# Optimization experiments

Measured on AMD Instinct MI355X. Metric: run time of the kernel, lower is better.

## Reference

```python
import jax, jax.numpy as jnp
import numpy as np

MAX_NUM_LEVELS = 3.5
NUM_LEVELS = 4  # mip levels 0..3 (levels clamped to [0, 2.5])


def affine_grid(matrix, N, H, W):
    # F.affine_grid, align_corners=False. matrix: (N,2,3) -> grid (N,H,W,2) in xy order.
    xs = (jnp.arange(W, dtype=jnp.float32) + 0.5) * (2.0 / W) - 1.0
    ys = (jnp.arange(H, dtype=jnp.float32) + 0.5) * (2.0 / H) - 1.0
    gy, gx = jnp.meshgrid(ys, xs, indexing='ij')
    base = jnp.stack([gx, gy, jnp.ones_like(gx)], axis=-1)  # (H,W,3)
    return jnp.einsum('hwk,nik->nhwi', base, matrix)  # (N,H,W,2)


def grid_sample_border(img, grid):
    # bilinear grid_sample, padding_mode='border', align_corners=False
    N, C, H, W = img.shape
    x = (grid[..., 0] + 1.0) * (W / 2.0) - 0.5
    y = (grid[..., 1] + 1.0) * (H / 2.0) - 0.5
    x0 = jnp.floor(x); y0 = jnp.floor(y)
    tx = x - x0; ty = y - y0
    x0i = jnp.clip(x0.astype(jnp.int32), 0, W - 1)
    x1i = jnp.clip(x0.astype(jnp.int32) + 1, 0, W - 1)
    y0i = jnp.clip(y0.astype(jnp.int32), 0, H - 1)
    y1i = jnp.clip(y0.astype(jnp.int32) + 1, 0, H - 1)
    b = jnp.arange(N)[:, None, None]
    g = lambda yi, xi: img[b, :, yi, xi]  # (N,Ho,Wo,C) gather
    out = (g(y0i, x0i) * ((1 - tx) * (1 - ty))[..., None]
           + g(y0i, x1i) * (tx * (1 - ty))[..., None]
           + g(y1i, x0i) * ((1 - tx) * ty)[..., None]
           + g(y1i, x1i) * (tx * ty)[..., None])
    return jnp.transpose(out, (0, 3, 1, 2))  # (N,C,Ho,Wo)


def blur_downsample(x):
    N, C, H, W = x.shape
    k1 = jnp.array([1., 3., 3., 1.], dtype=x.dtype) / 8.0
    k = k1[:, None] * k1[None, :]
    xp = jnp.pad(x, ((0, 0), (0, 0), (1, 2), (1, 2)), mode='reflect')
    kernel = jnp.broadcast_to(k[None, None], (C, 1, 4, 4))
    return jax.lax.conv_general_dilated(xp, kernel, window_strides=(2, 2), padding='VALID',
                                        feature_group_count=C,
                                        dimension_numbers=('NCHW', 'OIHW', 'NCHW'))


def compute_levels(grid, H, W):
    # per-pixel mip LOD from local stretch of the sampling grid (in source pixel units)
    coords = (grid + 1.0) * 0.5 * jnp.array([W, H], dtype=grid.dtype)  # (N,Ho,Wo,2)
    dx = coords[:, :-1, 1:] - coords[:, :-1, :-1]
    dy = coords[:, 1:, :-1] - coords[:, :-1, :-1]
    scale = jnp.maximum(jnp.linalg.norm(dx, axis=-1), jnp.linalg.norm(dy, axis=-1))
    scale = jnp.pad(scale, ((0, 0), (0, 1), (0, 1)), mode='edge')  # (N,Ho,Wo)
    levels = jnp.log2(jnp.maximum(scale, 1.0))
    return jnp.clip(levels, 0.0, MAX_NUM_LEVELS - 1.0)


def mipmap_warp(img, grid):
    N, C, H, W = img.shape
    levels = compute_levels(grid, H, W)  # (N,Ho,Wo)
    pyr = [img]
    for _ in range(NUM_LEVELS - 1):
        pyr.append(blur_downsample(pyr[-1]))
    samples = jnp.stack([grid_sample_border(p, grid) for p in pyr], axis=0)  # (L,N,C,Ho,Wo)
    ls = jnp.arange(NUM_LEVELS, dtype=levels.dtype)[:, None, None, None]
    w = jnp.clip(1.0 - jnp.abs(levels[None] - ls), 0.0, 1.0)  # trilinear blend weights (L,N,Ho,Wo)
    return jnp.einsum('lnhw,lnchw->nchw', w, samples)


def setup_inputs() -> dict:
    key = jax.random.key(0)
    k1, k2, k3 = jax.random.split(key, 3)
    N, C, H, W, D = 64, 3, 256, 256, 512
    img = jax.random.normal(k1, (N, C, H, W), dtype=jnp.float32)
    features = jax.random.normal(k2, (N, D), dtype=jnp.float32)
    # learned head params (zero-init in torch; small random here so the warp is nontrivial)
    lin_w = jax.random.normal(k3, (4, D), dtype=jnp.float32) * 0.02
    lin_b = jnp.zeros((4,), dtype=jnp.float32)
    return {'img': img, 'features': features, 'lin_w': lin_w, 'lin_b': lin_b}


def reference(img, features, lin_w, lin_b):
    params = features @ lin_w.T + lin_b  # (N,4)
    rot = jnp.tanh(params[:, 0:1]) * jnp.pi
    scale = jnp.exp(params[:, 1:2])
    sx, sy = params[:, 2:3], params[:, 3:4]
    c, s = jnp.cos(rot), jnp.sin(rot)
    matrix = jnp.concatenate([scale * c, -scale * s, sx, scale * s, scale * c, sy], axis=1).reshape(-1, 2, 3)
    affine_params = jnp.concatenate([rot, scale, sx, sy], axis=1)
    N, C, H, W = img.shape
    grid = affine_grid(matrix, N, H, W)
    out = mipmap_warp(img, grid)
    return out, grid, matrix, affine_params
```

## Files before the change

kernel.cpp:

```cpp
#include <hip/hip_runtime.h>
#include <math.h>

#define N_B 64
#define C_CH 3
#define H_IMG 256
#define W_IMG 256
#define D_FEAT 512

#define OUT_OFF_GRID   12582912
#define OUT_OFF_MATRIX 20971520
#define OUT_OFF_AFFINE 20971904

__global__ void params_kernel(const float* __restrict__ features,
                              const float* __restrict__ lin_w,
                              const float* __restrict__ lin_b,
                              float* __restrict__ out_matrix,
                              float* __restrict__ out_affine,
                              float* __restrict__ ws_params)
{
    const int n = blockIdx.x;
    const int t = threadIdx.x;
    const float* f = features + n * D_FEAT;
    float f0 = f[t];
    float f1 = f[t + 256];
    float a0 = f0 * lin_w[0 * D_FEAT + t] + f1 * lin_w[0 * D_FEAT + t + 256];
    float a1 = f0 * lin_w[1 * D_FEAT + t] + f1 * lin_w[1 * D_FEAT + t + 256];
    float a2 = f0 * lin_w[2 * D_FEAT + t] + f1 * lin_w[2 * D_FEAT + t + 256];
    float a3 = f0 * lin_w[3 * D_FEAT + t] + f1 * lin_w[3 * D_FEAT + t + 256];

    __shared__ float red[4][256];
    red[0][t] = a0; red[1][t] = a1; red[2][t] = a2; red[3][t] = a3;
    __syncthreads();
    for (int s = 128; s > 0; s >>= 1) {
        if (t < s) {
            red[0][t] += red[0][t + s];
            red[1][t] += red[1][t + s];
            red[2][t] += red[2][t + s];
            red[3][t] += red[3][t + s];
        }
        __syncthreads();
    }
    if (t == 0) {
        float p0 = red[0][0] + lin_b[0];
        float p1 = red[1][0] + lin_b[1];
        float p2 = red[2][0] + lin_b[2];
        float p3 = red[3][0] + lin_b[3];
        float rot   = tanhf(p0) * 3.14159265358979323846f;
        float scale = expf(p1);
        float c = cosf(rot), s = sinf(rot);
        float m00 = scale * c, m01 = -scale * s, m02 = p2;
        float m10 = scale * s, m11 =  scale * c, m12 = p3;
        out_matrix[n * 6 + 0] = m00;
        out_matrix[n * 6 + 1] = m01;
        out_matrix[n * 6 + 2] = m02;
        out_matrix[n * 6 + 3] = m10;
        out_matrix[n * 6 + 4] = m11;
        out_matrix[n * 6 + 5] = m12;
        out_affine[n * 4 + 0] = rot;
        out_affine[n * 4 + 1] = scale;
        out_affine[n * 4 + 2] = p2;
        out_affine[n * 4 + 3] = p3;
        float lv = log2f(fmaxf(scale, 1.0f));
        lv = fminf(fmaxf(lv, 0.0f), 2.5f);
        ws_params[n * 8 + 0] = m00;
        ws_params[n * 8 + 1] = m01;
        ws_params[n * 8 + 2] = m02;
        ws_params[n * 8 + 3] = m10;
        ws_params[n * 8 + 4] = m11;
        ws_params[n * 8 + 5] = m12;
        ws_params[n * 8 + 6] = lv;
        ws_params[n * 8 + 7] = 0.0f;
    }
}

template<int Hs, int Ws>
__global__ void down_kernel(const float* __restrict__ src, float* __restrict__ dst)
{
    constexpr int Hd = Hs / 2, Wd = Ws / 2;
    constexpr int QUADS = Wd / 4;

    const int idx = blockIdx.x * blockDim.x + threadIdx.x;
    const int t   = idx & (QUADS - 1);
    const int i   = (idx / QUADS) & (Hd - 1);
    const int nc  = idx / (QUADS * Hd);

    const float* __restrict__ s = src + (size_t)nc * Hs * Ws;

    int r[4];
#pragma unroll
    for (int a = 0; a < 4; a++) {
        int q = 2 * i + a - 1;
        if (q < 0) q = -q;
        if (q >= Hs) q = 2 * Hs - 2 - q;
        r[a] = q;
    }
    const int c8 = 8 * t;
    const int li = (t > 0)         ? c8 - 1 : 1;
    const int ri = (t < QUADS - 1) ? c8 + 8 : Ws - 2;

    const float k0 = 0.125f, k1 = 0.375f;
    const float kr[4] = {0.125f, 0.375f, 0.375f, 0.125f};

    float acc0 = 0.f, acc1 = 0.f, acc2 = 0.f, acc3 = 0.f;
#pragma unroll
    for (int a = 0; a < 4; a++) {
        const float* row = s + (size_t)r[a] * Ws;
        float4 A = *(const float4*)(row + c8);
        float4 B = *(const float4*)(row + c8 + 4);
        float L = row[li];
        float R = row[ri];
        float h0 = k0 * L   + k1 * A.x + k1 * A.y + k0 * A.z;
        float h1 = k0 * A.y + k1 * A.z + k1 * A.w + k0 * B.x;
        float h2 = k0 * A.w + k1 * B.x + k1 * B.y + k0 * B.z;
        float h3 = k0 * B.y + k1 * B.z + k1 * B.w + k0 * R;
        acc0 += kr[a] * h0;
        acc1 += kr[a] * h1;
        acc2 += kr[a] * h2;
        acc3 += kr[a] * h3;
    }
    float4* d4 = (float4*)(dst + (size_t)nc * Hd * Wd + (size_t)i * Wd + 4 * t);
    *d4 = make_float4(acc0, acc1, acc2, acc3);
}

__device__ __forceinline__ const float* lvl_ptr(int l, const float* img,
                                                const float* p1, const float* p2,
                                                const float* p3)
{
    return (l == 0) ? img : ((l == 1) ? p1 : ((l == 2) ? p2 : p3));
}

__device__ __forceinline__ void sample_level_pair(const float* __restrict__ p, int n, int l,
                                                  float X, float Y, float out[3])
{
    const int Wl = W_IMG >> l;
    const int Hl = H_IMG >> l;
    float x = (X + 1.0f) * (0.5f * (float)Wl) - 0.5f;
    float y = (Y + 1.0f) * (0.5f * (float)Hl) - 0.5f;
    float x0f = floorf(x), y0f = floorf(y);
    float tx = x - x0f, ty = y - y0f;
    int x0 = (int)x0f, y0 = (int)y0f;
    int y0i = min(max(y0,     0), Hl - 1);
    int y1i = min(max(y0 + 1, 0), Hl - 1);
    int xp = min(max(x0, 0), Wl - 2);
    const bool selHi0 = (x0 >= Wl - 1);
    const bool selLo1 = (x0 < 0);
    float w00 = (1.0f - tx) * (1.0f - ty);
    float w01 = tx * (1.0f - ty);
    float w10 = (1.0f - tx) * ty;
    float w11 = tx * ty;
    const float* base = p + (size_t)n * C_CH * Hl * Wl;
#pragma unroll
    for (int c = 0; c < C_CH; c++) {
        const float* pc = base + (size_t)c * Hl * Wl;
        float2 a = *(const float2*)(pc + y0i * Wl + xp);
        float2 b = *(const float2*)(pc + y1i * Wl + xp);
        float t00 = selHi0 ? a.y : a.x;
        float t01 = selLo1 ? a.x : a.y;
        float t10 = selHi0 ? b.y : b.x;
        float t11 = selLo1 ? b.x : b.y;
        out[c] = w00 * t00 + w01 * t01 + w10 * t10 + w11 * t11;
    }
}

__global__ void warp_kernel(const float* __restrict__ img,
                            const float* __restrict__ pyr1,
                            const float* __restrict__ pyr2,
                            const float* __restrict__ pyr3,
                            const float* __restrict__ ws_params,
                            float* __restrict__ out,
                            float* __restrict__ gridOut)
{
    const int n = blockIdx.y;
    const int tile = blockIdx.x;
    const int tid = threadIdx.x;
    const int w0 = (tile & 7) << 5;
    const int h0 = (tile >> 3) << 3;
    const int w = w0 + (((tid >> 6) & 1) << 4) + (tid & 15);
    const int h = h0 + ((tid >> 7) << 2) + ((tid >> 4) & 3);

    const float* P = ws_params + n * 8;
    float m00 = P[0], m01 = P[1], m02 = P[2];
    float m10 = P[3], m11 = P[4], m12 = P[5];
    float lv  = P[6];

    float gx = ((float)w + 0.5f) * (2.0f / (float)W_IMG) - 1.0f;
    float gy = ((float)h + 0.5f) * (2.0f / (float)H_IMG) - 1.0f;
    float X = m00 * gx + m01 * gy + m02;
    float Y = m10 * gx + m11 * gy + m12;

    float2* g2 = (float2*)gridOut + ((size_t)(n * H_IMG + h) * W_IMG + w);
    __builtin_nontemporal_store(X, &g2->x);
    __builtin_nontemporal_store(Y, &g2->y);

    int   l0   = (int)lv;
    float frac = lv - (float)l0;

    float c0[3];
    sample_level_pair(lvl_ptr(l0, img, pyr1, pyr2, pyr3), n, l0, X, Y, c0);

    float r0, r1, r2;
    if (frac > 0.0f) {
        float c1[3];
        sample_level_pair(lvl_ptr(l0 + 1, img, pyr1, pyr2, pyr3), n, l0 + 1, X, Y, c1);
        float wA = 1.0f - frac;
        r0 = wA * c0[0] + frac * c1[0];
        r1 = wA * c0[1] + frac * c1[1];
        r2 = wA * c0[2] + frac * c1[2];
    } else {
        r0 = c0[0]; r1 = c0[1]; r2 = c0[2];
    }

    size_t base = ((size_t)n * C_CH * H_IMG + h) * W_IMG + w;
    __builtin_nontemporal_store(r0, out + base);
    __builtin_nontemporal_store(r1, out + base + (size_t)H_IMG * W_IMG);
    __builtin_nontemporal_store(r2, out + base + (size_t)2 * H_IMG * W_IMG);
}

extern "C" void kernel_launch(void* const* d_in, const int* in_sizes, int n_in,
                              void* d_out, int out_size, void* d_ws, size_t ws_size,
                              hipStream_t stream)
{
    const float* img      = (const float*)d_in[0];
    const float* features = (const float*)d_in[1];
    const float* lin_w    = (const float*)d_in[2];
    const float* lin_b    = (const float*)d_in[3];

    float* out        = (float*)d_out;
    float* gridOut    = out + OUT_OFF_GRID;
    float* out_matrix = out + OUT_OFF_MATRIX;
    float* out_affine = out + OUT_OFF_AFFINE;

    float* ws        = (float*)d_ws;
    float* ws_params = ws;
    float* pyr1 = ws + 1024;
    float* pyr2 = pyr1 + (size_t)N_B * C_CH * 128 * 128;
    float* pyr3 = pyr2 + (size_t)N_B * C_CH * 64 * 64;

    params_kernel<<<N_B, 256, 0, stream>>>(features, lin_w, lin_b,
                                           out_matrix, out_affine, ws_params);

    int t1 = N_B * C_CH * 128 * 32;
    down_kernel<256, 256><<<t1 / 256, 256, 0, stream>>>(img,  pyr1);
    int t2 = N_B * C_CH * 64 * 16;
    down_kernel<128, 128><<<t2 / 256, 256, 0, stream>>>(pyr1, pyr2);
    int t3 = N_B * C_CH * 32 * 8;
    down_kernel<64, 64><<<t3 / 256, 256, 0, stream>>>(pyr2, pyr3);

    warp_kernel<<<dim3(H_IMG * W_IMG / 256, N_B), 256, 0, stream>>>(
        img, pyr1, pyr2, pyr3, ws_params, out, gridOut);
}
```

Measured before the change: 174.6 us.

## Skip unused pyramid levels per image and warp two pixels per thread

Each downsample kernel now reads the per-image mip level and returns early when that image never samples the level being built, so pyramid work for low-scale images is skipped. The warp kernel is restructured so each thread handles two horizontally adjacent pixels. The second grid coordinate is derived incrementally, grid output is written as one 16-byte store, and the channel outputs as 8-byte stores. The grid launch is halved to match. This trades extra registers per thread for fewer threads and wider memory transactions. The early exit also adds a divergent branch and a read of the parameters before any other work.

Result: slower. 181.7 us (+4.1%).

```diff
diff --git a/kernel.cpp b/kernel.cpp
--- a/kernel.cpp
+++ b/kernel.cpp
@@ -10,6 +10,9 @@
 #define OUT_OFF_GRID   12582912
 #define OUT_OFF_MATRIX 20971520
 #define OUT_OFF_AFFINE 20971904
+
+typedef float v4f __attribute__((ext_vector_type(4)));
+typedef float v2f __attribute__((ext_vector_type(2)));
 
 __global__ void params_kernel(const float* __restrict__ features,
                               const float* __restrict__ lin_w,
@@ -74,15 +77,20 @@
 }
 
 template<int Hs, int Ws>
-__global__ void down_kernel(const float* __restrict__ src, float* __restrict__ dst)
+__global__ void down_kernel(const float* __restrict__ src, float* __restrict__ dst,
+                            const float* __restrict__ ws_params, float lvl_gate)
 {
     constexpr int Hd = Hs / 2, Wd = Ws / 2;
     constexpr int QUADS = Wd / 4;
 
     const int idx = blockIdx.x * blockDim.x + threadIdx.x;
+    const int nc  = idx / (QUADS * Hd);
+    const int n   = nc / C_CH;
+
+    if (ws_params[n * 8 + 6] <= lvl_gate) return;
+
     const int t   = idx & (QUADS - 1);
     const int i   = (idx / QUADS) & (Hd - 1);
-    const int nc  = idx / (QUADS * Hd);
 
     const float* __restrict__ s = src + (size_t)nc * Hs * Ws;
 
@@ -129,7 +137,7 @@
     return (l == 0) ? img : ((l == 1) ? p1 : ((l == 2) ? p2 : p3));
 }
 
-__device__ __forceinline__ void sample_level_pair(const float* __restrict__ p, int n, int l,
+__device__ __forceinline__ void sample_level_pair(const float* __restrict__ base, int l,
                                                   float X, float Y, float out[3])
 {
     const int Wl = W_IMG >> l;
@@ -148,7 +156,6 @@
     float w01 = tx * (1.0f - ty);
     float w10 = (1.0f - tx) * ty;
     float w11 = tx * ty;
-    const float* base = p + (size_t)n * C_CH * Hl * Wl;
 #pragma unroll
     for (int c = 0; c < C_CH; c++) {
         const float* pc = base + (size_t)c * Hl * Wl;
@@ -170,50 +177,66 @@
                             float* __restrict__ out,
                             float* __restrict__ gridOut)
 {
-    const int n = blockIdx.y;
+    const int n    = blockIdx.y;
     const int tile = blockIdx.x;
-    const int tid = threadIdx.x;
-    const int w0 = (tile & 7) << 5;
-    const int h0 = (tile >> 3) << 3;
-    const int w = w0 + (((tid >> 6) & 1) << 4) + (tid & 15);
-    const int h = h0 + ((tid >> 7) << 2) + ((tid >> 4) & 3);
+    const int tid  = threadIdx.x;
+    const int w0 = (tile & 3) << 6;
+    const int h0 = (tile >> 2) << 3;
+    const int w  = w0 + ((tid & 31) << 1);
+    const int h  = h0 + (tid >> 5);
 
     const float* P = ws_params + n * 8;
     float m00 = P[0], m01 = P[1], m02 = P[2];
     float m10 = P[3], m11 = P[4], m12 = P[5];
     float lv  = P[6];
 
-    float gx = ((float)w + 0.5f) * (2.0f / (float)W_IMG) - 1.0f;
+    const float STEP = 2.0f / (float)W_IMG;
+    float gx = ((float)w + 0.5f) * STEP - 1.0f;
     float gy = ((float)h + 0.5f) * (2.0f / (float)H_IMG) - 1.0f;
-    float X = m00 * gx + m01 * gy + m02;
-    float Y = m10 * gx + m11 * gy + m12;
-
-    float2* g2 = (float2*)gridOut + ((size_t)(n * H_IMG + h) * W_IMG + w);
-    __builtin_nontemporal_store(X, &g2->x);
-    __builtin_nontemporal_store(Y, &g2->y);
+    float X0 = m00 * gx + m01 * gy + m02;
+    float Y0 = m10 * gx + m11 * gy + m12;
+    float X1 = X0 + m00 * STEP;
+    float Y1 = Y0 + m10 * STEP;
+
+    v4f gq = {X0, Y0, X1, Y1};
+    v4f* g4 = (v4f*)gridOut + (((size_t)(n * H_IMG + h) * W_IMG + w) >> 1);
+    __builtin_nontemporal_store(gq, g4);
 
     int   l0   = (int)lv;
     float frac = lv - (float)l0;
 
-    float c0[3];
-    sample_level_pair(lvl_ptr(l0, img, pyr1, pyr2, pyr3), n, l0, X, Y, c0);
-
-    float r0, r1, r2;
+    const int Wl0 = W_IMG >> l0,       Hl0 = H_IMG >> l0;
+    const int Wl1 = W_IMG >> (l0 + 1), Hl1 = H_IMG >> (l0 + 1);
+    const float* base0 = lvl_ptr(l0, img, pyr1, pyr2, pyr3) + (size_t)n * C_CH * Hl0 * Wl0;
+
+    float a0[3], b0[3];
+    sample_level_pair(base0, l0, X0, Y0, a0);
+    sample_level_pair(base0, l0, X1, Y1, b0);
+
+    float rA[3], rB[3];
     if (frac > 0.0f) {
-        float c1[3];
-        sample_level_pair(lvl_ptr(l0 + 1, img, pyr1, pyr2, pyr3), n, l0 + 1, X, Y, c1);
+        const float* base1 = lvl_ptr(l0 + 1, img, pyr1, pyr2, pyr3)
+                           + (size_t)n * C_CH * Hl1 * Wl1;
+        float a1[3], b1[3];
+        sample_level_pair(base1, l0 + 1, X0, Y0, a1);
+        sample_level_pair(base1, l0 + 1, X1, Y1, b1);
         float wA = 1.0f - frac;
-        r0 = wA * c0[0] + frac * c1[0];
-        r1 = wA * c0[1] + frac * c1[1];
-        r2 = wA * c0[2] + frac * c1[2];
+#pragma unroll
+        for (int c = 0; c < C_CH; c++) {
+            rA[c] = wA * a0[c] + frac * a1[c];
+            rB[c] = wA * b0[c] + frac * b1[c];
+        }
     } else {
-        r0 = c0[0]; r1 = c0[1]; r2 = c0[2];
+#pragma unroll
+        for (int c = 0; c < C_CH; c++) { rA[c] = a0[c]; rB[c] = b0[c]; }
     }
 
     size_t base = ((size_t)n * C_CH * H_IMG + h) * W_IMG + w;
-    __builtin_nontemporal_store(r0, out + base);
-    __builtin_nontemporal_store(r1, out + base + (size_t)H_IMG * W_IMG);
-    __builtin_nontemporal_store(r2, out + base + (size_t)2 * H_IMG * W_IMG);
+#pragma unroll
+    for (int c = 0; c < C_CH; c++) {
+        v2f o = {rA[c], rB[c]};
+        __builtin_nontemporal_store(o, (v2f*)(out + base + (size_t)c * H_IMG * W_IMG));
+    }
 }
 
 extern "C" void kernel_launch(void* const* d_in, const int* in_sizes, int n_in,
@@ -240,12 +263,12 @@
                                            out_matrix, out_affine, ws_params);
 
     int t1 = N_B * C_CH * 128 * 32;
-    down_kernel<256, 256><<<t1 / 256, 256, 0, stream>>>(img,  pyr1);
+    down_kernel<256, 256><<<t1 / 256, 256, 0, stream>>>(img,  pyr1, ws_params, 0.0f);
     int t2 = N_B * C_CH * 64 * 16;
-    down_kernel<128, 128><<<t2 / 256, 256, 0, stream>>>(pyr1, pyr2);
+    down_kernel<128, 128><<<t2 / 256, 256, 0, stream>>>(pyr1, pyr2, ws_params, 1.0f);
     int t3 = N_B * C_CH * 32 * 8;
-    down_kernel<64, 64><<<t3 / 256, 256, 0, stream>>>(pyr2, pyr3);
-
-    warp_kernel<<<dim3(H_IMG * W_IMG / 256, N_B), 256, 0, stream>>>(
+    down_kernel<64, 64><<<t3 / 256, 256, 0, stream>>>(pyr2, pyr3, ws_params, 2.0f);
+
+    warp_kernel<<<dim3(128, N_B), 256, 0, stream>>>(
         img, pyr1, pyr2, pyr3, ws_params, out, gridOut);
 }
```
